# Optimization experiments

Hardware: AMD Instinct MI355X
Metric: run time of the kernel (lower is better)

Reference implementation:

```python
import jax, jax.numpy as jnp
from jax import lax
import numpy as np

SEQ = 1024
VOCAB = 50000
EMB = 300
CAS_V, CAS_D = 8, 50
POS_V, POS_D = 48, 50
IN_DIM = EMB + CAS_D + POS_D  # 400
H = 512
T = 13  # num_classes / CRF tags


def setup_inputs() -> dict:
    key = jax.random.key(0)
    ks = jax.random.split(key, 16)
    s = lambda k, shape, sc=0.05: jax.random.normal(k, shape, dtype=jnp.float32) * sc
    return {
        "x": jax.random.randint(ks[0], (SEQ,), 0, VOCAB),
        "casing": jax.random.randint(ks[1], (SEQ,), 0, CAS_V),
        "pos": jax.random.randint(ks[2], (SEQ,), 0, POS_V),
        "h0": jnp.zeros((2, H), dtype=jnp.float32),
        "c0": jnp.zeros((2, H), dtype=jnp.float32),
        "W_emb": s(ks[3], (VOCAB, EMB)),
        "W_cas": s(ks[4], (CAS_V, CAS_D)),
        "W_pos": s(ks[5], (POS_V, POS_D)),
        "Wx_f": s(ks[6], (IN_DIM, 4 * H)),
        "Wh_f": s(ks[7], (H, 4 * H)),
        "b_f": jnp.zeros((4 * H,), dtype=jnp.float32),
        "Wx_b": s(ks[8], (IN_DIM, 4 * H)),
        "Wh_b": s(ks[9], (H, 4 * H)),
        "b_b": jnp.zeros((4 * H,), dtype=jnp.float32),
        "W_out": s(ks[10], (2 * H, T)),
        "b_out": jnp.zeros((T,), dtype=jnp.float32),
        "trans": s(ks[11], (T, T), 0.1),
        "start_trans": s(ks[12], (T,), 0.1),
        "end_trans": s(ks[13], (T,), 0.1),
    }


def _lstm_dir(feat, Wx, Wh, b, h0, c0, reverse):
    # feat: [L, IN_DIM]; precompute input projection for all steps
    pre = feat @ Wx + b  # [L, 4H]

    def step(carry, p):
        h, c = carry
        z = p + h @ Wh
        i, f, g, o = jnp.split(z, 4, axis=-1)
        c = jax.nn.sigmoid(f) * c + jax.nn.sigmoid(i) * jnp.tanh(g)
        h = jax.nn.sigmoid(o) * jnp.tanh(c)
        return (h, c), h

    _, hs = lax.scan(step, (h0, c0), pre, reverse=reverse)
    return hs  # [L, H]


def _viterbi(em, trans, start_trans, end_trans):
    # em: [L, T] emission (log) scores; max-plus DP
    score0 = start_trans + em[0]

    def fwd(score, e):
        total = score[:, None] + trans  # [T, T]: prev -> next
        best = jnp.max(total, axis=0) + e
        idx = jnp.argmax(total, axis=0)
        return best, idx

    final, hist = lax.scan(fwd, score0, em[1:])  # hist: [L-1, T]
    final = final + end_trans
    last = jnp.argmax(final)

    def back(tag, idx_row):
        return idx_row[tag], tag

    first, rest = lax.scan(back, last, hist, reverse=True)
    return jnp.concatenate([first[None], rest])  # [L] int


def reference(x, casing, pos, h0, c0, W_emb, W_cas, W_pos, Wx_f, Wh_f, b_f,
              Wx_b, Wh_b, b_b, W_out, b_out, trans, start_trans, end_trans):
    # AWD-LSTM encode (eval mode: dropout identity)
    feat = jnp.concatenate([W_emb[x], W_cas[casing], W_pos[pos]], axis=-1)  # [L, 400]
    hf = _lstm_dir(feat, Wx_f, Wh_f, b_f, h0[0], c0[0], reverse=False)
    hb = _lstm_dir(feat, Wx_b, Wh_b, b_b, h0[1], c0[1], reverse=True)
    o = jnp.concatenate([hf, hb], axis=-1) @ W_out + b_out  # [L, T]
    tag_scores = jax.nn.log_softmax(o, axis=1)
    path = _viterbi(tag_scores, trans, start_trans, end_trans)
    return tag_scores, path
```

## Files before the change

kernel.cpp:

```cpp
#include <hip/hip_runtime.h>
#include <hip/hip_bf16.h>
#include <math.h>

#define SEQ 1024
#define HID 512
#define FOURH 2048
#define IND 400
#define NT 13

#define NWG_DIR 32
#define LSTM_THREADS 512
#define JPW 16
#define WCOLS 64
#define TAG_INVALID 0xFFFFFFFFu

__device__ __forceinline__ float bf2f(unsigned short u) {
    union { unsigned u32; float f; } v;
    v.u32 = ((unsigned)u) << 16;
    return v.f;
}

__device__ __forceinline__ unsigned short f2bf(float f) {
    union { float f; unsigned u; } v;
    v.f = f;
    unsigned u = v.u;
    unsigned rounding = 0x7FFFu + ((u >> 16) & 1u);
    u += rounding;
    return (unsigned short)(u >> 16);
}

__device__ __forceinline__ float ldf(const void* p, size_t i, int isf32) {
    return isf32 ? ((const float*)p)[i] : bf2f(((const unsigned short*)p)[i]);
}

__device__ __forceinline__ float fsigm(float x) {
    return __builtin_amdgcn_rcpf(1.f + __builtin_amdgcn_exp2f(-1.44269504f * x));
}
__device__ __forceinline__ float ftanhf(float x) {
    return 1.f - 2.f * __builtin_amdgcn_rcpf(__builtin_amdgcn_exp2f(2.88539008f * x) + 1.f);
}
__device__ __forceinline__ float satz(float z) { return fminf(fmaxf(z, -60.f), 60.f); }

__global__ __launch_bounds__(64) void detect_kernel(const unsigned short* __restrict__ w,
                                                    int* __restrict__ flag,
                                                    unsigned* __restrict__ vcnt) {
    int lane = threadIdx.x;
    int cnt = 0;
    for (int i = 0; i < 4; ++i) {
        unsigned short u = w[2 * (lane * 4 + i)];
        int e = (u >> 7) & 0xFF;
        if (e >= 90 && e < 127) cnt++;
    }
#pragma unroll
    for (int off = 32; off >= 1; off >>= 1) cnt += __shfl_xor(cnt, off, 64);
    if (lane == 0) *flag = (cnt < 128) ? 1 : 0;
    if (lane == 1) *vcnt = 0;
}

__global__ __launch_bounds__(256) void pre_gemm_kernel(
        const int* __restrict__ x, const int* __restrict__ cas, const int* __restrict__ pos,
        const void* __restrict__ W_emb, const void* __restrict__ W_cas, const void* __restrict__ W_pos,
        const void* __restrict__ Wx_f, const void* __restrict__ b_f,
        const void* __restrict__ Wx_b, const void* __restrict__ b_b,
        unsigned short* __restrict__ pre, const int* __restrict__ dflag) {
    __shared__ float ftile[32 * IND];
    __shared__ int idxs[96];
    const int isf32 = *dflag;
    int dir = blockIdx.z;
    const void* Wx = dir ? Wx_b : Wx_f;
    const void* bb = dir ? b_b : b_f;
    unsigned short* pre_d = pre + (size_t)dir * SEQ * FOURH;
    int r0 = blockIdx.y * 32;
    int col = blockIdx.x * 256 + threadIdx.x;
    int tid = threadIdx.x;

    if (tid < 32)       idxs[tid] = x[r0 + tid];
    else if (tid < 64)  idxs[tid] = cas[r0 + tid - 32];
    else if (tid < 96)  idxs[tid] = pos[r0 + tid - 64];
    __syncthreads();

    for (int idx = tid; idx < 32 * IND; idx += 256) {
        int r = idx / IND;
        int e = idx - r * IND;
        float v;
        if (e < 300)      v = ldf(W_emb, (size_t)idxs[r] * 300 + e, isf32);
        else if (e < 350) v = ldf(W_cas, (size_t)idxs[32 + r] * 50 + (e - 300), isf32);
        else              v = ldf(W_pos, (size_t)idxs[64 + r] * 50 + (e - 350), isf32);
        ftile[idx] = v;
    }
    __syncthreads();

    float acc[32];
    float bias = ldf(bb, col, isf32);
#pragma unroll
    for (int r = 0; r < 32; ++r) acc[r] = bias;

    if (isf32) {
        const float* W = (const float*)Wx;
        for (int kk = 0; kk < 100; ++kk) {
            int k = kk * 4;
            float w0 = W[(size_t)(k + 0) * FOURH + col];
            float w1 = W[(size_t)(k + 1) * FOURH + col];
            float w2 = W[(size_t)(k + 2) * FOURH + col];
            float w3 = W[(size_t)(k + 3) * FOURH + col];
#pragma unroll
            for (int r = 0; r < 32; ++r) {
                float4 f = *(const float4*)&ftile[r * IND + k];
                acc[r] += f.x * w0 + f.y * w1 + f.z * w2 + f.w * w3;
            }
        }
    } else {
        const unsigned short* W = (const unsigned short*)Wx;
        for (int kk = 0; kk < 100; ++kk) {
            int k = kk * 4;
            float w0 = bf2f(W[(size_t)(k + 0) * FOURH + col]);
            float w1 = bf2f(W[(size_t)(k + 1) * FOURH + col]);
            float w2 = bf2f(W[(size_t)(k + 2) * FOURH + col]);
            float w3 = bf2f(W[(size_t)(k + 3) * FOURH + col]);
#pragma unroll
            for (int r = 0; r < 32; ++r) {
                float4 f = *(const float4*)&ftile[r * IND + k];
                acc[r] += f.x * w0 + f.y * w1 + f.z * w2 + f.w * w3;
            }
        }
    }
    for (int r = 0; r < 32; ++r) pre_d[(size_t)(r0 + r) * FOURH + col] = f2bf(acc[r]);
}

__global__ __launch_bounds__(LSTM_THREADS, 2) void lstm_kernel(
        const void* __restrict__ Wh_f, const void* __restrict__ Wh_b,
        const void* __restrict__ h0, const void* __restrict__ c0,
        const unsigned short* __restrict__ pre, float* __restrict__ hsout,
        unsigned long long* hbuf, const int* __restrict__ dflag) {
    __shared__ float red[2][8 * WCOLS];

    const int isf32 = *dflag;
    const int tid = threadIdx.x;
    const int b = blockIdx.x;
    const int dir = b & 1;
    const int g = b >> 1;
    const int j0 = g * JPW;

    const void* Wh = dir ? Wh_b : Wh_f;
    const unsigned short* pre_d = pre + (size_t)dir * SEQ * FOURH;
    float* hso = hsout + (size_t)dir * SEQ * HID;
    unsigned long long* hb_d  = hbuf + dir * 2 * HID;
    unsigned long long* hb2_d = hbuf + 4096 + dir * 2 * HID;

    const int seg  = tid >> 6;
    const int col  = tid & 63;
    const int unit = col & 15;
    const int gate = col >> 4;
    const int gcol = gate * HID + j0 + unit;
    const int redoff = seg * WCOLS + unit * 4 + gate;

    const int isep  = (tid < 64);
    const int eunit = tid >> 2;
    const int egate = tid & 3;
    const int ispub = isep && (egate == 0);

    float4 w0, w1, w2, w3, w4, w5, w6, w7, w8, w9, w10, w11, w12, w13, w14, w15;
    if (isf32) {
        const float* wp = (const float*)Wh + (size_t)(seg * 64) * FOURH + gcol;
#define LDW(i) w##i = make_float4(wp[(size_t)(4*i+0)*FOURH], wp[(size_t)(4*i+1)*FOURH], \
                                  wp[(size_t)(4*i+2)*FOURH], wp[(size_t)(4*i+3)*FOURH])
        LDW(0); LDW(1); LDW(2); LDW(3); LDW(4); LDW(5); LDW(6); LDW(7);
        LDW(8); LDW(9); LDW(10); LDW(11); LDW(12); LDW(13); LDW(14); LDW(15);
#undef LDW
    } else {
        const unsigned short* wp = (const unsigned short*)Wh + (size_t)(seg * 64) * FOURH + gcol;
#define LDW(i) w##i = make_float4(bf2f(wp[(size_t)(4*i+0)*FOURH]), bf2f(wp[(size_t)(4*i+1)*FOURH]), \
                                  bf2f(wp[(size_t)(4*i+2)*FOURH]), bf2f(wp[(size_t)(4*i+3)*FOURH]))
        LDW(0); LDW(1); LDW(2); LDW(3); LDW(4); LDW(5); LDW(6); LDW(7);
        LDW(8); LDW(9); LDW(10); LDW(11); LDW(12); LDW(13); LDW(14); LDW(15);
#undef LDW
    }

    float creg = 0.f;
    unsigned short zn = 0;
    if (isep) {
        if (ispub) {
            creg = ldf(c0, dir * HID + j0 + eunit, isf32);
            float h0v = ldf(h0, dir * HID + j0 + eunit, isf32);
            unsigned long long wv = (unsigned long long)__float_as_uint(h0v);
            unsigned long long iv = ((unsigned long long)TAG_INVALID << 32);
            __hip_atomic_store(&hb_d[j0 + eunit],        wv, __ATOMIC_RELAXED, __HIP_MEMORY_SCOPE_AGENT);
            __hip_atomic_store(&hb2_d[j0 + eunit],       wv, __ATOMIC_RELAXED, __HIP_MEMORY_SCOPE_AGENT);
            __hip_atomic_store(&hb_d[HID + j0 + eunit],  iv, __ATOMIC_RELAXED, __HIP_MEMORY_SCOPE_AGENT);
            __hip_atomic_store(&hb2_d[HID + j0 + eunit], iv, __ATOMIC_RELAXED, __HIP_MEMORY_SCOPE_AGENT);
        }
        int t0 = dir ? (SEQ - 1) : 0;
        zn = pre_d[(size_t)t0 * FOURH + egate * HID + j0 + eunit];
    }
    __syncthreads();

    for (int s = 0; s < SEQ; ++s) {
        const int t = dir ? (SEQ - 1 - s) : s;

        unsigned hu;
        {
            const unsigned long long* A = &hb_d[(s & 1) * HID + tid];
            const unsigned long long* B = &hb2_d[(s & 1) * HID + tid];
            const unsigned expect = (unsigned)s;
            unsigned long long va = __hip_atomic_load(A, __ATOMIC_RELAXED, __HIP_MEMORY_SCOPE_AGENT);
            unsigned long long vb = __hip_atomic_load(B, __ATOMIC_RELAXED, __HIP_MEMORY_SCOPE_AGENT);
            for (;;) {
                if ((unsigned)(va >> 32) == expect) { hu = (unsigned)va; break; }
                va = __hip_atomic_load(A, __ATOMIC_RELAXED, __HIP_MEMORY_SCOPE_AGENT);
                if ((unsigned)(vb >> 32) == expect) { hu = (unsigned)vb; break; }
                vb = __hip_atomic_load(B, __ATOMIC_RELAXED, __HIP_MEMORY_SCOPE_AGENT);
            }
        }

        float zc = 0.f;
        if (isep) {
            zc = bf2f(zn);
            if (s + 1 < SEQ) {
                int tn = dir ? (SEQ - 2 - s) : (s + 1);
                zn = pre_d[(size_t)tn * FOURH + egate * HID + j0 + eunit];
            }
        }

        float a0 = 0.f, a1 = 0.f, a2 = 0.f, a3 = 0.f;
#define MACQ(i, A) { \
        float hx = __uint_as_float((unsigned)__builtin_amdgcn_readlane((int)hu, 4*i+0)); \
        float hy = __uint_as_float((unsigned)__builtin_amdgcn_readlane((int)hu, 4*i+1)); \
        float hz = __uint_as_float((unsigned)__builtin_amdgcn_readlane((int)hu, 4*i+2)); \
        float hw = __uint_as_float((unsigned)__builtin_amdgcn_readlane((int)hu, 4*i+3)); \
        A += hx * w##i.x + hy * w##i.y + hz * w##i.z + hw * w##i.w; }
        MACQ(0, a0)  MACQ(1, a1)  MACQ(2, a2)  MACQ(3, a3)
        MACQ(4, a0)  MACQ(5, a1)  MACQ(6, a2)  MACQ(7, a3)
        MACQ(8, a0)  MACQ(9, a1)  MACQ(10, a2) MACQ(11, a3)
        MACQ(12, a0) MACQ(13, a1) MACQ(14, a2) MACQ(15, a3)
#undef MACQ
        red[s & 1][redoff] = (a0 + a1) + (a2 + a3);
        __syncthreads();

        if (isep) {
            const float* rp = &red[s & 1][0];
            float z = rp[0 * WCOLS + tid] + rp[1 * WCOLS + tid]
                    + rp[2 * WCOLS + tid] + rp[3 * WCOLS + tid]
                    + rp[4 * WCOLS + tid] + rp[5 * WCOLS + tid]
                    + rp[6 * WCOLS + tid] + rp[7 * WCOLS + tid];
            z = satz(z + zc);
            float vs = fsigm(z);
            float vt = ftanhf(z);
            float v = (egate == 2) ? vt : vs;
            float x1 = __shfl_xor(v, 1, 64);
            float x2 = __shfl_xor(v, 2, 64);
            float x3 = __shfl_xor(x1, 2, 64);
            if (ispub) {
                float ig = v, fg = x1, gg = x2, og = x3;
                float cnew = fg * creg + ig * gg;
                creg = cnew;
                float hnew = og * ftanhf(satz(cnew));
                unsigned long long w = ((unsigned long long)(unsigned)(s + 1) << 32)
                                     | (unsigned long long)__float_as_uint(hnew);
                const int par = (s + 1) & 1;
                __hip_atomic_store(&hb_d[par * HID + j0 + eunit], w,
                                   __ATOMIC_RELAXED, __HIP_MEMORY_SCOPE_AGENT);
                __hip_atomic_store(&hb2_d[par * HID + j0 + eunit], w,
                                   __ATOMIC_RELAXED, __HIP_MEMORY_SCOPE_AGENT);
                hso[(size_t)t * HID + j0 + eunit] = hnew;
            }
        }
    }
}

__global__ __launch_bounds__(64) void outproj_kernel(const float* __restrict__ hsout,
        const void* __restrict__ W_out, const void* __restrict__ b_out,
        float* __restrict__ out_scores,
        const void* __restrict__ trans, const void* __restrict__ strans,
        const void* __restrict__ etrans, float* __restrict__ out_path,
        unsigned* __restrict__ vcnt, const int* __restrict__ dflag) {
    __shared__ unsigned char hist[SEQ][NT];
    const int isf32 = *dflag;
    int t = blockIdx.x;
    int lane = threadIdx.x;
    const float* hf = hsout + (size_t)t * HID;
    const float* hb = hsout + (size_t)SEQ * HID + (size_t)t * HID;
    float acc[NT];
#pragma unroll
    for (int j = 0; j < NT; ++j) acc[j] = 0.f;
    for (int k = lane; k < HID; k += 64) {
        float a = hf[k], b2 = hb[k];
#pragma unroll
        for (int j = 0; j < NT; ++j)
            acc[j] += a * ldf(W_out, (size_t)k * NT + j, isf32)
                    + b2 * ldf(W_out, (size_t)(HID + k) * NT + j, isf32);
    }
#pragma unroll
    for (int off = 32; off >= 1; off >>= 1) {
#pragma unroll
        for (int j = 0; j < NT; ++j) acc[j] += __shfl_xor(acc[j], off, 64);
    }
    float o[NT];
    float m = -1e30f;
#pragma unroll
    for (int j = 0; j < NT; ++j) { o[j] = acc[j] + ldf(b_out, j, isf32); m = fmaxf(m, o[j]); }
    float lse = 0.f;
#pragma unroll
    for (int j = 0; j < NT; ++j) lse += expf(o[j] - m);
    lse = m + logf(lse);
    if (lane < NT)
        __hip_atomic_store(&out_scores[t * NT + lane], o[lane] - lse,
                           __ATOMIC_RELAXED, __HIP_MEMORY_SCOPE_AGENT);
    __builtin_amdgcn_s_waitcnt(0);

    unsigned old = 0;
    if (lane == 0) old = atomicAdd(vcnt, 1u);
    old = __shfl(old, 0, 64);
    if (old != SEQ - 1) return;

    const float* em = out_scores;
    int j = lane < NT ? lane : 0;
    float tr[NT];
#pragma unroll
    for (int i = 0; i < NT; ++i) tr[i] = ldf(trans, i * NT + j, isf32);
#define EML(tt) __hip_atomic_load(&em[(size_t)(tt) * NT + j], __ATOMIC_RELAXED, __HIP_MEMORY_SCOPE_AGENT)
    float score = ldf(strans, j, isf32) + EML(0);
    float c0 = EML(1), c1 = EML(2), c2 = EML(3), c3 = EML(4),
          c4 = EML(5), c5 = EML(6), c6 = EML(7), c7 = EML(8);
#define VSTEP(PE, TT) { \
    float best = -1e30f; int arg = 0; \
    _Pragma("unroll") \
    for (int i = 0; i < NT; ++i) { \
        float si = __shfl(score, i, 64); \
        float cand = si + tr[i]; \
        if (cand > best) { best = cand; arg = i; } \
    } \
    if (lane < NT) hist[TT][lane] = (unsigned char)arg; \
    score = best + PE; }
    for (int tb = 1; tb < SEQ; tb += 8) {
        int nb = tb + 8;
        float n0 = 0.f, n1 = 0.f, n2 = 0.f, n3 = 0.f, n4 = 0.f, n5 = 0.f, n6 = 0.f, n7 = 0.f;
        if (nb + 0 < SEQ) n0 = EML(nb + 0);
        if (nb + 1 < SEQ) n1 = EML(nb + 1);
        if (nb + 2 < SEQ) n2 = EML(nb + 2);
        if (nb + 3 < SEQ) n3 = EML(nb + 3);
        if (nb + 4 < SEQ) n4 = EML(nb + 4);
        if (nb + 5 < SEQ) n5 = EML(nb + 5);
        if (nb + 6 < SEQ) n6 = EML(nb + 6);
        if (nb + 7 < SEQ) n7 = EML(nb + 7);
        VSTEP(c0, tb + 0)
        if (tb + 1 < SEQ) VSTEP(c1, tb + 1)
        if (tb + 2 < SEQ) VSTEP(c2, tb + 2)
        if (tb + 3 < SEQ) VSTEP(c3, tb + 3)
        if (tb + 4 < SEQ) VSTEP(c4, tb + 4)
        if (tb + 5 < SEQ) VSTEP(c5, tb + 5)
        if (tb + 6 < SEQ) VSTEP(c6, tb + 6)
        if (tb + 7 < SEQ) VSTEP(c7, tb + 7)
        c0 = n0; c1 = n1; c2 = n2; c3 = n3; c4 = n4; c5 = n5; c6 = n6; c7 = n7;
    }
#undef VSTEP
#undef EML
    score += ldf(etrans, j, isf32);
    float bmax = -1e30f;
    int last = 0;
#pragma unroll
    for (int i = 0; i < NT; ++i) {
        float si = __shfl(score, i, 64);
        if (si > bmax) { bmax = si; last = i; }
    }
    if (lane == 0) {
        int cur = last;
        out_path[SEQ - 1] = (float)cur;
        for (int tt = SEQ - 1; tt >= 1; --tt) {
            cur = hist[tt][cur];
            out_path[tt - 1] = (float)cur;
        }
    }
}

extern "C" void kernel_launch(void* const* d_in, const int* in_sizes, int n_in,
                              void* d_out, int out_size, void* d_ws, size_t ws_size,
                              hipStream_t stream) {
    const int* x      = (const int*)d_in[0];
    const int* casing = (const int*)d_in[1];
    const int* posi   = (const int*)d_in[2];
    const void* h0    = d_in[3];
    const void* c0    = d_in[4];
    const void* W_emb = d_in[5];
    const void* W_cas = d_in[6];
    const void* W_pos = d_in[7];
    const void* Wx_f  = d_in[8];
    const void* Wh_f  = d_in[9];
    const void* b_f   = d_in[10];
    const void* Wx_b  = d_in[11];
    const void* Wh_b  = d_in[12];
    const void* b_b   = d_in[13];
    const void* W_out = d_in[14];
    const void* b_out = d_in[15];
    const void* trans = d_in[16];
    const void* strans = d_in[17];
    const void* etrans = d_in[18];

    char* ws = (char*)d_ws;
    int* dflag          = (int*)(ws + 448);
    unsigned* vcnt      = (unsigned*)(ws + 456);
    unsigned short* pre = (unsigned short*)(ws + 512);
    float* hsout        = (float*)(ws + 512 + 8388608);
    unsigned long long* hbuf = (unsigned long long*)(ws + 512 + 8388608 + 4194304);

    float* out_scores = (float*)d_out;
    float* out_path   = out_scores + SEQ * NT;

    detect_kernel<<<1, 64, 0, stream>>>((const unsigned short*)W_emb, dflag, vcnt);

    dim3 g2(8, 32, 2);
    pre_gemm_kernel<<<g2, 256, 0, stream>>>(x, casing, posi, W_emb, W_cas, W_pos,
                                            Wx_f, b_f, Wx_b, b_b, pre, dflag);

    lstm_kernel<<<2 * NWG_DIR, LSTM_THREADS, 0, stream>>>(
        Wh_f, Wh_b, h0, c0, pre, hsout, hbuf, dflag);

    outproj_kernel<<<SEQ, 64, 0, stream>>>(hsout, W_out, b_out, out_scores,
                                           trans, strans, etrans, out_path, vcnt, dflag);
}
```

Before: 2.281 ms.

## Fuse input-projection GEMM into LSTM kernel with per-tile ready flags

Merges the input projection GEMM and the recurrent LSTM into one launch. Blocks beyond the first 64 compute 32-row tiles of the projection, ordered from both sequence ends, and publish each tile by bumping a per-direction, per-row-block counter. The LSTM blocks spin on that counter before reading pre-activations, so the recurrence can start while later tiles are still being computed, hiding the GEMM latency and one launch. The risks are spin-wait deadlock if the LSTM blocks are not co-resident with the producers, contention between GEMM blocks and the latency-bound recurrence, and the extra cost of packed atomic stores.

```diff
diff --git a/kernel.cpp b/kernel.cpp
--- a/kernel.cpp
+++ b/kernel.cpp
@@ -8,8 +8,8 @@
 #define IND 400
 #define NT 13
 
-#define NWG_DIR 32
-#define LSTM_THREADS 512
+#define LSTM_WGS 64
+#define NGEMM 256
 #define JPW 16
 #define WCOLS 64
 #define TAG_INVALID 0xFFFFFFFFu
@@ -43,7 +43,8 @@
 
 __global__ __launch_bounds__(64) void detect_kernel(const unsigned short* __restrict__ w,
                                                     int* __restrict__ flag,
-                                                    unsigned* __restrict__ vcnt) {
+                                                    unsigned* __restrict__ vcnt,
+                                                    unsigned* __restrict__ flags) {
     int lane = threadIdx.x;
     int cnt = 0;
     for (int i = 0; i < 4; ++i) {
@@ -55,94 +56,111 @@
     for (int off = 32; off >= 1; off >>= 1) cnt += __shfl_xor(cnt, off, 64);
     if (lane == 0) *flag = (cnt < 128) ? 1 : 0;
     if (lane == 1) *vcnt = 0;
-}
-
-__global__ __launch_bounds__(256) void pre_gemm_kernel(
+    flags[lane] = 0;
+}
+
+__global__ __launch_bounds__(512, 2) void fused_kernel(
         const int* __restrict__ x, const int* __restrict__ cas, const int* __restrict__ pos,
         const void* __restrict__ W_emb, const void* __restrict__ W_cas, const void* __restrict__ W_pos,
         const void* __restrict__ Wx_f, const void* __restrict__ b_f,
         const void* __restrict__ Wx_b, const void* __restrict__ b_b,
-        unsigned short* __restrict__ pre, const int* __restrict__ dflag) {
-    __shared__ float ftile[32 * IND];
-    __shared__ int idxs[96];
-    const int isf32 = *dflag;
-    int dir = blockIdx.z;
-    const void* Wx = dir ? Wx_b : Wx_f;
-    const void* bb = dir ? b_b : b_f;
-    unsigned short* pre_d = pre + (size_t)dir * SEQ * FOURH;
-    int r0 = blockIdx.y * 32;
-    int col = blockIdx.x * 256 + threadIdx.x;
-    int tid = threadIdx.x;
-
-    if (tid < 32)       idxs[tid] = x[r0 + tid];
-    else if (tid < 64)  idxs[tid] = cas[r0 + tid - 32];
-    else if (tid < 96)  idxs[tid] = pos[r0 + tid - 64];
-    __syncthreads();
-
-    for (int idx = tid; idx < 32 * IND; idx += 256) {
-        int r = idx / IND;
-        int e = idx - r * IND;
-        float v;
-        if (e < 300)      v = ldf(W_emb, (size_t)idxs[r] * 300 + e, isf32);
-        else if (e < 350) v = ldf(W_cas, (size_t)idxs[32 + r] * 50 + (e - 300), isf32);
-        else              v = ldf(W_pos, (size_t)idxs[64 + r] * 50 + (e - 350), isf32);
-        ftile[idx] = v;
-    }
-    __syncthreads();
-
-    float acc[32];
-    float bias = ldf(bb, col, isf32);
-#pragma unroll
-    for (int r = 0; r < 32; ++r) acc[r] = bias;
-
-    if (isf32) {
-        const float* W = (const float*)Wx;
-        for (int kk = 0; kk < 100; ++kk) {
-            int k = kk * 4;
-            float w0 = W[(size_t)(k + 0) * FOURH + col];
-            float w1 = W[(size_t)(k + 1) * FOURH + col];
-            float w2 = W[(size_t)(k + 2) * FOURH + col];
-            float w3 = W[(size_t)(k + 3) * FOURH + col];
-#pragma unroll
-            for (int r = 0; r < 32; ++r) {
-                float4 f = *(const float4*)&ftile[r * IND + k];
-                acc[r] += f.x * w0 + f.y * w1 + f.z * w2 + f.w * w3;
-            }
-        }
-    } else {
-        const unsigned short* W = (const unsigned short*)Wx;
-        for (int kk = 0; kk < 100; ++kk) {
-            int k = kk * 4;
-            float w0 = bf2f(W[(size_t)(k + 0) * FOURH + col]);
-            float w1 = bf2f(W[(size_t)(k + 1) * FOURH + col]);
-            float w2 = bf2f(W[(size_t)(k + 2) * FOURH + col]);
-            float w3 = bf2f(W[(size_t)(k + 3) * FOURH + col]);
-#pragma unroll
-            for (int r = 0; r < 32; ++r) {
-                float4 f = *(const float4*)&ftile[r * IND + k];
-                acc[r] += f.x * w0 + f.y * w1 + f.z * w2 + f.w * w3;
-            }
-        }
-    }
-    for (int r = 0; r < 32; ++r) pre_d[(size_t)(r0 + r) * FOURH + col] = f2bf(acc[r]);
-}
-
-__global__ __launch_bounds__(LSTM_THREADS, 2) void lstm_kernel(
         const void* __restrict__ Wh_f, const void* __restrict__ Wh_b,
         const void* __restrict__ h0, const void* __restrict__ c0,
-        const unsigned short* __restrict__ pre, float* __restrict__ hsout,
-        unsigned long long* hbuf, const int* __restrict__ dflag) {
-    __shared__ float red[2][8 * WCOLS];
-
+        unsigned long long* __restrict__ preu, float* __restrict__ hsout,
+        unsigned long long* hbuf, const int* __restrict__ dflag,
+        unsigned* __restrict__ flags) {
+    __shared__ float smem[12800 + 96];
     const int isf32 = *dflag;
     const int tid = threadIdx.x;
     const int b = blockIdx.x;
+
+    if (b >= LSTM_WGS) {
+        const int e = b - LSTM_WGS;
+        const int gdir = e & 1;
+        const int rest = e >> 1;
+        const int bx = rest & 3;
+        const int byi = rest >> 2;
+        const int by = (byi & 1) ? (31 - (byi >> 1)) : (byi >> 1);
+        const void* Wx = gdir ? Wx_b : Wx_f;
+        const void* bb = gdir ? b_b : b_f;
+        const int r0 = by * 32;
+        const int col = bx * 512 + tid;
+        float* ftile = smem;
+        int* idxs = (int*)&smem[12800];
+
+        if (tid < 32)       idxs[tid] = x[r0 + tid];
+        else if (tid < 64)  idxs[tid] = cas[r0 + tid - 32];
+        else if (tid < 96)  idxs[tid] = pos[r0 + tid - 64];
+        __syncthreads();
+
+        for (int idx = tid; idx < 32 * IND; idx += 512) {
+            int r = idx / IND;
+            int el = idx - r * IND;
+            float v;
+            if (el < 300)      v = ldf(W_emb, (size_t)idxs[r] * 300 + el, isf32);
+            else if (el < 350) v = ldf(W_cas, (size_t)idxs[32 + r] * 50 + (el - 300), isf32);
+            else               v = ldf(W_pos, (size_t)idxs[64 + r] * 50 + (el - 350), isf32);
+            ftile[idx] = v;
+        }
+        __syncthreads();
+
+        float acc[32];
+        float bias = ldf(bb, col, isf32);
+#pragma unroll
+        for (int r = 0; r < 32; ++r) acc[r] = bias;
+
+        if (isf32) {
+            const float* W = (const float*)Wx;
+            for (int kk = 0; kk < 100; ++kk) {
+                int k = kk * 4;
+                float w0 = W[(size_t)(k + 0) * FOURH + col];
+                float w1 = W[(size_t)(k + 1) * FOURH + col];
+                float w2 = W[(size_t)(k + 2) * FOURH + col];
+                float w3 = W[(size_t)(k + 3) * FOURH + col];
+#pragma unroll
+                for (int r = 0; r < 32; ++r) {
+                    float4 f = *(const float4*)&ftile[r * IND + k];
+                    acc[r] += f.x * w0 + f.y * w1 + f.z * w2 + f.w * w3;
+                }
+            }
+        } else {
+            const unsigned short* W = (const unsigned short*)Wx;
+            for (int kk = 0; kk < 100; ++kk) {
+                int k = kk * 4;
+                float w0 = bf2f(W[(size_t)(k + 0) * FOURH + col]);
+                float w1 = bf2f(W[(size_t)(k + 1) * FOURH + col]);
+                float w2 = bf2f(W[(size_t)(k + 2) * FOURH + col]);
+                float w3 = bf2f(W[(size_t)(k + 3) * FOURH + col]);
+#pragma unroll
+                for (int r = 0; r < 32; ++r) {
+                    float4 f = *(const float4*)&ftile[r * IND + k];
+                    acc[r] += f.x * w0 + f.y * w1 + f.z * w2 + f.w * w3;
+                }
+            }
+        }
+
+        unsigned long long* dst = preu + (size_t)gdir * SEQ * (FOURH / 4);
+        for (int r = 0; r < 32; ++r) {
+            unsigned long long w = ((unsigned long long)f2bf(acc[r])) << (16 * (tid & 3));
+            w |= __shfl_xor(w, 1, 64);
+            w |= __shfl_xor(w, 2, 64);
+            if ((tid & 3) == 0)
+                __hip_atomic_store(&dst[(size_t)(r0 + r) * 512 + (col >> 2)], w,
+                                   __ATOMIC_RELAXED, __HIP_MEMORY_SCOPE_AGENT);
+        }
+        asm volatile("s_waitcnt vmcnt(0)" ::: "memory");
+        __syncthreads();
+        if (tid == 0) atomicAdd(&flags[gdir * 32 + by], 1u);
+        return;
+    }
+
+    float* redp = smem;
     const int dir = b & 1;
     const int g = b >> 1;
     const int j0 = g * JPW;
 
     const void* Wh = dir ? Wh_b : Wh_f;
-    const unsigned short* pre_d = pre + (size_t)dir * SEQ * FOURH;
+    const unsigned long long* preu_d = preu + (size_t)dir * SEQ * 512;
     float* hso = hsout + (size_t)dir * SEQ * HID;
     unsigned long long* hb_d  = hbuf + dir * 2 * HID;
     unsigned long long* hb2_d = hbuf + 4096 + dir * 2 * HID;
@@ -158,6 +176,8 @@
     const int eunit = tid >> 2;
     const int egate = tid & 3;
     const int ispub = isep && (egate == 0);
+    const int sub   = eunit & 3;
+    const int widx  = egate * 128 + ((j0 + eunit) >> 2);
 
     float4 w0, w1, w2, w3, w4, w5, w6, w7, w8, w9, w10, w11, w12, w13, w14, w15;
     if (isf32) {
@@ -177,7 +197,8 @@
     }
 
     float creg = 0.f;
-    unsigned short zn = 0;
+    unsigned long long znw = 0;
+    int curby = dir ? 31 : 0;
     if (isep) {
         if (ispub) {
             creg = ldf(c0, dir * HID + j0 + eunit, isf32);
@@ -189,8 +210,13 @@
             __hip_atomic_store(&hb_d[HID + j0 + eunit],  iv, __ATOMIC_RELAXED, __HIP_MEMORY_SCOPE_AGENT);
             __hip_atomic_store(&hb2_d[HID + j0 + eunit], iv, __ATOMIC_RELAXED, __HIP_MEMORY_SCOPE_AGENT);
         }
+        {
+            const unsigned* fp = &flags[dir * 32 + curby];
+            while (__hip_atomic_load(fp, __ATOMIC_RELAXED, __HIP_MEMORY_SCOPE_AGENT) < 4u) {}
+        }
         int t0 = dir ? (SEQ - 1) : 0;
-        zn = pre_d[(size_t)t0 * FOURH + egate * HID + j0 + eunit];
+        znw = __hip_atomic_load(&preu_d[(size_t)t0 * 512 + widx],
+                                __ATOMIC_RELAXED, __HIP_MEMORY_SCOPE_AGENT);
     }
     __syncthreads();
 
@@ -214,10 +240,17 @@
 
         float zc = 0.f;
         if (isep) {
-            zc = bf2f(zn);
+            zc = bf2f((unsigned short)(znw >> (16 * sub)));
             if (s + 1 < SEQ) {
                 int tn = dir ? (SEQ - 2 - s) : (s + 1);
-                zn = pre_d[(size_t)tn * FOURH + egate * HID + j0 + eunit];
+                int byn = tn >> 5;
+                if (byn != curby) {
+                    const unsigned* fp = &flags[dir * 32 + byn];
+                    while (__hip_atomic_load(fp, __ATOMIC_RELAXED, __HIP_MEMORY_SCOPE_AGENT) < 4u) {}
+                    curby = byn;
+                }
+                znw = __hip_atomic_load(&preu_d[(size_t)tn * 512 + widx],
+                                        __ATOMIC_RELAXED, __HIP_MEMORY_SCOPE_AGENT);
             }
         }
 
@@ -233,11 +266,11 @@
         MACQ(8, a0)  MACQ(9, a1)  MACQ(10, a2) MACQ(11, a3)
         MACQ(12, a0) MACQ(13, a1) MACQ(14, a2) MACQ(15, a3)
 #undef MACQ
-        red[s & 1][redoff] = (a0 + a1) + (a2 + a3);
+        redp[(s & 1) * 512 + redoff] = (a0 + a1) + (a2 + a3);
         __syncthreads();
 
         if (isep) {
-            const float* rp = &red[s & 1][0];
+            const float* rp = &redp[(s & 1) * 512];
             float z = rp[0 * WCOLS + tid] + rp[1 * WCOLS + tid]
                     + rp[2 * WCOLS + tid] + rp[3 * WCOLS + tid]
                     + rp[4 * WCOLS + tid] + rp[5 * WCOLS + tid]
@@ -398,21 +431,19 @@
     char* ws = (char*)d_ws;
     int* dflag          = (int*)(ws + 448);
     unsigned* vcnt      = (unsigned*)(ws + 456);
-    unsigned short* pre = (unsigned short*)(ws + 512);
+    unsigned long long* preu = (unsigned long long*)(ws + 512);
     float* hsout        = (float*)(ws + 512 + 8388608);
     unsigned long long* hbuf = (unsigned long long*)(ws + 512 + 8388608 + 4194304);
+    unsigned* flags     = (unsigned*)(ws + 512 + 8388608 + 4194304 + 65536);
 
     float* out_scores = (float*)d_out;
     float* out_path   = out_scores + SEQ * NT;
 
-    detect_kernel<<<1, 64, 0, stream>>>((const unsigned short*)W_emb, dflag, vcnt);
-
-    dim3 g2(8, 32, 2);
-    pre_gemm_kernel<<<g2, 256, 0, stream>>>(x, casing, posi, W_emb, W_cas, W_pos,
-                                            Wx_f, b_f, Wx_b, b_b, pre, dflag);
-
-    lstm_kernel<<<2 * NWG_DIR, LSTM_THREADS, 0, stream>>>(
-        Wh_f, Wh_b, h0, c0, pre, hsout, hbuf, dflag);
+    detect_kernel<<<1, 64, 0, stream>>>((const unsigned short*)W_emb, dflag, vcnt, flags);
+
+    fused_kernel<<<LSTM_WGS + NGEMM, 512, 0, stream>>>(
+        x, casing, posi, W_emb, W_cas, W_pos, Wx_f, b_f, Wx_b, b_b,
+        Wh_f, Wh_b, h0, c0, preu, hsout, hbuf, dflag, flags);
 
     outproj_kernel<<<SEQ, 64, 0, stream>>>(hsout, W_out, b_out, out_scores,
                                            trans, strans, etrans, out_path, vcnt, dflag);
```

New measurement: 2.305 ms. About the same (+1.0%).
